# Performance work log

Measured on AMD Instinct MI355X. Metric: run time of the kernel, lower is better.

The kernel has to match this reference:

```python
import jax, jax.numpy as jnp
import numpy as np


def _conv1x1_prelu(x, w, b, a):
    # 1x1 conv == channel matmul; PReLU with shared scalar slope a
    y = jnp.einsum('oc,nchw->nohw', w, x) + b[None, :, None, None]
    return jnp.where(y >= 0, y, a * y)


def setup_inputs() -> dict:
    key = jax.random.key(0)
    ks = jax.random.split(key, 7)
    N, C, H, W = 2, 128, 96, 96
    Ce = 64  # channel // reduction
    s_in = 1.0 / np.sqrt(C)
    return {
        'input': jax.random.normal(ks[0], (N, C, H, W), jnp.float32),
        'w1': jax.random.normal(ks[1], (Ce, C), jnp.float32) * s_in,
        'b1': jnp.zeros((Ce,), jnp.float32),
        'a1': jnp.full((1,), 0.25, jnp.float32),
        'w2': jax.random.normal(ks[2], (Ce, C), jnp.float32) * s_in,
        'b2': jnp.zeros((Ce,), jnp.float32),
        'a2': jnp.full((1,), 0.25, jnp.float32),
        'wa': jax.random.normal(ks[3], (C, C), jnp.float32) * s_in,
        'ba': jnp.zeros((C,), jnp.float32),
        'aa': jnp.full((1,), 0.25, jnp.float32),
    }


def reference(input, w1, b1, a1, w2, b2, a2, wa, ba, aa):
    e1 = _conv1x1_prelu(input, w1, b1, a1[0])  # [N, Ce, H, W]
    e2 = _conv1x1_prelu(input, w2, b2, a2[0])  # [N, Ce, H, W]
    xa = _conv1x1_prelu(input, wa, ba, aa[0])  # [N, C,  H, W]
    N, Ce, H, W = e1.shape
    HW = H * W
    q = e1.transpose(0, 2, 3, 1).reshape(N, HW, Ce)   # [N, HW, Ce]
    k = e2.reshape(N, Ce, HW)                          # [N, Ce, HW]
    score = jax.nn.softmax(jnp.matmul(q, k), axis=-1)  # [N, HW, HW] (no scale, as in source)
    v = xa.reshape(N, -1, HW).transpose(0, 2, 1)       # [N, HW, C]
    out = jnp.matmul(score, v)                         # [N, HW, C]
    return out.transpose(0, 2, 1).reshape(N, -1, H, W)
```

## Files before the change

kernel.cpp:

```cpp
#include <hip/hip_runtime.h>
#include <cstdint>
#include <cstddef>

#define HW_ 9216
#define CC 128
#define NQT 144
#define NQT2 72
#define LOG2E 1.44269504088896f

typedef short bf16x8 __attribute__((ext_vector_type(8)));
typedef unsigned short u16x4 __attribute__((ext_vector_type(4)));
typedef unsigned short u16x8 __attribute__((ext_vector_type(8)));
typedef float f32x4 __attribute__((ext_vector_type(4)));

__device__ __forceinline__ unsigned short f2bf(float f) {
    unsigned int u = __builtin_bit_cast(unsigned int, f);
    u += 0x7FFFu + ((u >> 16) & 1u);
    return (unsigned short)(u >> 16);
}

__device__ __forceinline__ float fast_exp2(float x) {
#if __has_builtin(__builtin_amdgcn_exp2f)
    return __builtin_amdgcn_exp2f(x);
#else
    return exp2f(x);
#endif
}

__device__ __forceinline__ unsigned int cvt_pk_bf16(float lo, float hi) {
    unsigned int r;
    asm("v_cvt_pk_bf16_f32 %0, %1, %2" : "=v"(r) : "v"(lo), "v"(hi));
    return r;
}

__global__ __launch_bounds__(256) void prep_w(const float* __restrict__ w1,
                                              const float* __restrict__ w2,
                                              const float* __restrict__ wa,
                                              float* __restrict__ wt) {
    int idx = blockIdx.x * 256 + threadIdx.x;
    int o = idx >> 7, c = idx & 127;
    float v;
    if (o < 64)       v = w1[o * 128 + c];
    else if (o < 128) v = w2[(o - 64) * 128 + c];
    else              v = wa[(o - 128) * 128 + c];
    wt[c * 256 + o] = v;
}

__global__ __launch_bounds__(256) void conv_kernel(
    const float* __restrict__ x, const float* __restrict__ wt,
    const float* __restrict__ b1, const float* __restrict__ a1,
    const float* __restrict__ b2, const float* __restrict__ a2,
    const float* __restrict__ ba, const float* __restrict__ aa,
    unsigned short* __restrict__ qb, unsigned short* __restrict__ kb,
    unsigned short* __restrict__ vtb) {
    const int ptile = blockIdx.x;
    const int oset  = blockIdx.y;
    const int n     = blockIdx.z;
    const int t = threadIdx.x;
    const int p = t & 63;
    const int og = __builtin_amdgcn_readfirstlane(t >> 6);
    const int p0 = ptile * 64;

    __shared__ float xs[128 * 64];
    for (int c = t >> 6; c < 128; c += 4)
        xs[c * 64 + p] = x[((size_t)n * CC + c) * HW_ + p0 + p];
    __syncthreads();

    const int obase = oset * 64 + og * 16;
    float acc[16];
#pragma unroll
    for (int i = 0; i < 16; i++) acc[i] = 0.f;

    for (int c = 0; c < 128; c++) {
        float xv = xs[c * 64 + p];
        const float* wr = wt + c * 256 + obase;
#pragma unroll
        for (int i = 0; i < 16; i++) acc[i] = fmaf(wr[i], xv, acc[i]);
    }

    const float* bias_p;
    const float* slope_p;
    if (oset == 0)      { bias_p = b1; slope_p = a1; }
    else if (oset == 1) { bias_p = b2; slope_p = a2; }
    else                { bias_p = ba; slope_p = aa; }
    const float slope = slope_p[0];

    unsigned short vals[16];
#pragma unroll
    for (int i = 0; i < 16; i++) {
        float bv = (oset < 2) ? bias_p[og * 16 + i] : bias_p[obase - 128 + i];
        float y = acc[i] + bv;
        y = (y >= 0.f) ? y : slope * y;
        if (oset == 0) y *= LOG2E;
        vals[i] = f2bf(y);
    }

    if (oset < 2) {
        unsigned short* dst = (oset == 0 ? qb : kb) + ((size_t)n * HW_ + p0 + p) * 64 + og * 16;
        bf16x8 v0, v1;
#pragma unroll
        for (int i = 0; i < 8; i++) { v0[i] = (short)vals[i]; v1[i] = (short)vals[8 + i]; }
        *(bf16x8*)(dst)     = v0;
        *(bf16x8*)(dst + 8) = v1;
    } else {
        int c0 = obase - 128;
#pragma unroll
        for (int i = 0; i < 16; i++)
            vtb[((size_t)n * CC + c0 + i) * HW_ + p0 + p] = vals[i];
    }
}

__global__ __launch_bounds__(256, 2) void attn_kernel(
    const unsigned short* __restrict__ qb, const unsigned short* __restrict__ kb,
    const unsigned short* __restrict__ vtb,
    float* __restrict__ o_part, float* __restrict__ l_part,
    int nch, int chunk_j) {
    const int qt    = blockIdx.x;
    const int chunk = blockIdx.y;
    const int n     = blockIdx.z;
    const int t = threadIdx.x;
    const int w = t >> 6;
    const int lane = t & 63;
    const int l15 = lane & 15;
    const int quad = lane >> 4;
    const int e7 = l15 & 7;

    __shared__ __align__(16) unsigned short k_lds[64 * 64];
    __shared__ __align__(16) unsigned short v_lds[128 * 64];
    __shared__ __align__(16) unsigned short p_lds[4 * 1024];

    const int row_ga = qt * 128 + w * 32 + l15;
    const int row_gb = row_ga + 16;
    const bf16x8 bq0a = *(const bf16x8*)(qb + ((size_t)n * HW_ + row_ga) * 64 + quad * 8);
    const bf16x8 bq1a = *(const bf16x8*)(qb + ((size_t)n * HW_ + row_ga) * 64 + 32 + quad * 8);
    const bf16x8 bq0b = *(const bf16x8*)(qb + ((size_t)n * HW_ + row_gb) * 64 + quad * 8);
    const bf16x8 bq1b = *(const bf16x8*)(qb + ((size_t)n * HW_ + row_gb) * 64 + 32 + quad * 8);

    f32x4 acc_oa[8], acc_ob[8];
#pragma unroll
    for (int i = 0; i < 8; i++) {
        acc_oa[i] = (f32x4){0.f, 0.f, 0.f, 0.f};
        acc_ob[i] = (f32x4){0.f, 0.f, 0.f, 0.f};
    }
    float l_sa = 0.f, l_sb = 0.f;

    const int stg_row = t >> 3, stg_seg = t & 7;
    const int iters = chunk_j / 64;
    int j0 = chunk * chunk_j;

    bf16x8 kr0, kr1, vr0, vr1, vr2, vr3;
    {
        const unsigned short* kp = kb + ((size_t)n * HW_ + j0 + stg_row) * 64 + stg_seg * 8;
        kr0 = *(const bf16x8*)kp;
        kr1 = *(const bf16x8*)(kp + 32 * 64);
        const unsigned short* vp = vtb + ((size_t)n * CC + stg_row) * HW_ + j0 + stg_seg * 8;
        vr0 = *(const bf16x8*)vp;
        vr1 = *(const bf16x8*)(vp + (size_t)32 * HW_);
        vr2 = *(const bf16x8*)(vp + (size_t)64 * HW_);
        vr3 = *(const bf16x8*)(vp + (size_t)96 * HW_);
    }

    for (int it = 0; it < iters; ++it, j0 += 64) {
        __syncthreads();
        {
            int r0 = stg_row, r1 = stg_row + 32;
            *(bf16x8*)&k_lds[r0 * 64 + ((stg_seg ^ (r0 & 7)) * 8)] = kr0;
            *(bf16x8*)&k_lds[r1 * 64 + ((stg_seg ^ (r1 & 7)) * 8)] = kr1;
            *(bf16x8*)&v_lds[r0 * 64 + ((stg_seg ^ (r0 & 7)) * 8)] = vr0;
            *(bf16x8*)&v_lds[r1 * 64 + ((stg_seg ^ (r1 & 7)) * 8)] = vr1;
            int r2 = stg_row + 64, r3 = stg_row + 96;
            *(bf16x8*)&v_lds[r2 * 64 + ((stg_seg ^ (r2 & 7)) * 8)] = vr2;
            *(bf16x8*)&v_lds[r3 * 64 + ((stg_seg ^ (r3 & 7)) * 8)] = vr3;
        }
        __syncthreads();

        if (it + 1 < iters) {
            const unsigned short* kp = kb + ((size_t)n * HW_ + j0 + 64 + stg_row) * 64 + stg_seg * 8;
            kr0 = *(const bf16x8*)kp;
            kr1 = *(const bf16x8*)(kp + 32 * 64);
            const unsigned short* vp = vtb + ((size_t)n * CC + stg_row) * HW_ + j0 + 64 + stg_seg * 8;
            vr0 = *(const bf16x8*)vp;
            vr1 = *(const bf16x8*)(vp + (size_t)32 * HW_);
            vr2 = *(const bf16x8*)(vp + (size_t)64 * HW_);
            vr3 = *(const bf16x8*)(vp + (size_t)96 * HW_);
        }

        f32x4 sa[4], sb[4];
#pragma unroll
        for (int ct = 0; ct < 4; ct++) {
            int jr = ct * 16 + l15;
            bf16x8 ak0 = *(const bf16x8*)&k_lds[jr * 64 + ((quad ^ e7) * 8)];
            bf16x8 ak1 = *(const bf16x8*)&k_lds[jr * 64 + (((4 + quad) ^ e7) * 8)];
            f32x4 za = (f32x4){0.f, 0.f, 0.f, 0.f};
            za = __builtin_amdgcn_mfma_f32_16x16x32_bf16(ak0, bq0a, za, 0, 0, 0);
            za = __builtin_amdgcn_mfma_f32_16x16x32_bf16(ak1, bq1a, za, 0, 0, 0);
            sa[ct] = za;
            f32x4 zb = (f32x4){0.f, 0.f, 0.f, 0.f};
            zb = __builtin_amdgcn_mfma_f32_16x16x32_bf16(ak0, bq0b, zb, 0, 0, 0);
            zb = __builtin_amdgcn_mfma_f32_16x16x32_bf16(ak1, bq1b, zb, 0, 0, 0);
            sb[ct] = zb;
        }

#pragma unroll
        for (int ct = 0; ct < 4; ct++) {
            sa[ct][0] = fast_exp2(sa[ct][0]);
            sa[ct][1] = fast_exp2(sa[ct][1]);
            sa[ct][2] = fast_exp2(sa[ct][2]);
            sa[ct][3] = fast_exp2(sa[ct][3]);
        }
        {
            float u0 = sa[0][0] + sa[0][1], u1 = sa[0][2] + sa[0][3];
            float u2 = sa[1][0] + sa[1][1], u3 = sa[1][2] + sa[1][3];
            float u4 = sa[2][0] + sa[2][1], u5 = sa[2][2] + sa[2][3];
            float u6 = sa[3][0] + sa[3][1], u7 = sa[3][2] + sa[3][3];
            float v0 = u0 + u1, v1 = u2 + u3, v2 = u4 + u5, v3 = u6 + u7;
            l_sa += (v0 + v1) + (v2 + v3);
        }
#pragma unroll
        for (int ct = 0; ct < 4; ct++) {
            unsigned int pk01 = cvt_pk_bf16(sa[ct][0], sa[ct][1]);
            unsigned int pk23 = cvt_pk_bf16(sa[ct][2], sa[ct][3]);
            int chunkid = 2 * ct + (quad >> 1);
            int off = l15 * 64 + ((chunkid ^ e7) * 8) + 4 * (quad & 1);
            uint2 tmp;
            tmp.x = pk01;
            tmp.y = pk23;
            *(u16x4*)&p_lds[w * 1024 + off] = __builtin_bit_cast(u16x4, tmp);
        }
        asm volatile("" ::: "memory");
        const bf16x8 bp0a = __builtin_bit_cast(bf16x8,
            *(const u16x8*)&p_lds[w * 1024 + l15 * 64 + ((quad ^ e7) * 8)]);
        const bf16x8 bp1a = __builtin_bit_cast(bf16x8,
            *(const u16x8*)&p_lds[w * 1024 + l15 * 64 + (((4 + quad) ^ e7) * 8)]);
        asm volatile("" ::: "memory");

#pragma unroll
        for (int ct = 0; ct < 4; ct++) {
            sb[ct][0] = fast_exp2(sb[ct][0]);
            sb[ct][1] = fast_exp2(sb[ct][1]);
            sb[ct][2] = fast_exp2(sb[ct][2]);
            sb[ct][3] = fast_exp2(sb[ct][3]);
        }
        {
            float u0 = sb[0][0] + sb[0][1], u1 = sb[0][2] + sb[0][3];
            float u2 = sb[1][0] + sb[1][1], u3 = sb[1][2] + sb[1][3];
            float u4 = sb[2][0] + sb[2][1], u5 = sb[2][2] + sb[2][3];
            float u6 = sb[3][0] + sb[3][1], u7 = sb[3][2] + sb[3][3];
            float v0 = u0 + u1, v1 = u2 + u3, v2 = u4 + u5, v3 = u6 + u7;
            l_sb += (v0 + v1) + (v2 + v3);
        }
#pragma unroll
        for (int ct = 0; ct < 4; ct++) {
            unsigned int pk01 = cvt_pk_bf16(sb[ct][0], sb[ct][1]);
            unsigned int pk23 = cvt_pk_bf16(sb[ct][2], sb[ct][3]);
            int chunkid = 2 * ct + (quad >> 1);
            int off = l15 * 64 + ((chunkid ^ e7) * 8) + 4 * (quad & 1);
            uint2 tmp;
            tmp.x = pk01;
            tmp.y = pk23;
            *(u16x4*)&p_lds[w * 1024 + off] = __builtin_bit_cast(u16x4, tmp);
        }
        asm volatile("" ::: "memory");
        const bf16x8 bp0b = __builtin_bit_cast(bf16x8,
            *(const u16x8*)&p_lds[w * 1024 + l15 * 64 + ((quad ^ e7) * 8)]);
        const bf16x8 bp1b = __builtin_bit_cast(bf16x8,
            *(const u16x8*)&p_lds[w * 1024 + l15 * 64 + (((4 + quad) ^ e7) * 8)]);
        asm volatile("" ::: "memory");

        __builtin_amdgcn_s_setprio(1);
#pragma unroll
        for (int ctv = 0; ctv < 8; ctv++) {
            int cr = ctv * 16 + l15;
            bf16x8 av0 = *(const bf16x8*)&v_lds[cr * 64 + ((quad ^ e7) * 8)];
            bf16x8 av1 = *(const bf16x8*)&v_lds[cr * 64 + (((4 + quad) ^ e7) * 8)];
            acc_oa[ctv] = __builtin_amdgcn_mfma_f32_16x16x32_bf16(av0, bp0a, acc_oa[ctv], 0, 0, 0);
            acc_oa[ctv] = __builtin_amdgcn_mfma_f32_16x16x32_bf16(av1, bp1a, acc_oa[ctv], 0, 0, 0);
            acc_ob[ctv] = __builtin_amdgcn_mfma_f32_16x16x32_bf16(av0, bp0b, acc_ob[ctv], 0, 0, 0);
            acc_ob[ctv] = __builtin_amdgcn_mfma_f32_16x16x32_bf16(av1, bp1b, acc_ob[ctv], 0, 0, 0);
        }
        __builtin_amdgcn_s_setprio(0);
    }

    l_sa += __shfl_xor(l_sa, 16);
    l_sa += __shfl_xor(l_sa, 32);
    l_sb += __shfl_xor(l_sb, 16);
    l_sb += __shfl_xor(l_sb, 32);

    const size_t cbase = ((size_t)(n * NQT2 + qt) * nch + chunk) * 128;
    const int qla = w * 32 + l15, qlb = qla + 16;
#pragma unroll
    for (int ctv = 0; ctv < 8; ctv++)
#pragma unroll
        for (int r = 0; r < 4; r++) {
            int c = ctv * 16 + 4 * quad + r;
            o_part[(cbase + c) * 128 + qla] = acc_oa[ctv][r];
            o_part[(cbase + c) * 128 + qlb] = acc_ob[ctv][r];
        }
    if (quad == 0) {
        size_t lb = ((size_t)(n * NQT2 + qt) * nch + chunk) * 128;
        l_part[lb + qla] = l_sa;
        l_part[lb + qlb] = l_sb;
    }
}

__global__ __launch_bounds__(256) void combine_kernel(
    const float* __restrict__ o_part, const float* __restrict__ lp,
    float* __restrict__ out, int nch) {
    int gid = blockIdx.x * 256 + threadIdx.x;
    int r = gid & 127;
    int rest = gid >> 7;
    int c = rest & 127;
    int nqt = rest >> 7;
    int n = nqt / NQT2, qtp = nqt - n * NQT2;

    float num = 0.f, den = 0.f;
    for (int ch = 0; ch < nch; ch++) {
        num += o_part[(((size_t)nqt * nch + ch) * 128 + c) * 128 + r];
        den += lp[((size_t)nqt * nch + ch) * 128 + r];
    }
    out[((size_t)n * CC + c) * HW_ + qtp * 128 + r] = num / den;
}

extern "C" void kernel_launch(void* const* d_in, const int* in_sizes, int n_in,
                              void* d_out, int out_size, void* d_ws, size_t ws_size,
                              hipStream_t stream) {
    const float* x  = (const float*)d_in[0];
    const float* w1 = (const float*)d_in[1];
    const float* b1 = (const float*)d_in[2];
    const float* a1 = (const float*)d_in[3];
    const float* w2 = (const float*)d_in[4];
    const float* b2 = (const float*)d_in[5];
    const float* a2 = (const float*)d_in[6];
    const float* wa = (const float*)d_in[7];
    const float* ba = (const float*)d_in[8];
    const float* aa = (const float*)d_in[9];
    float* out = (float*)d_out;

    auto need = [](int nc) -> size_t {
        return 9568256ull + (size_t)nc * 9437184ull + (size_t)nc * 73728ull;
    };
    int nch;
    if (ws_size >= need(12))     nch = 12;
    else if (ws_size >= need(8)) nch = 8;
    else if (ws_size >= need(6)) nch = 6;
    else if (ws_size >= need(4)) nch = 4;
    else                         nch = 2;
    const int chunk_j = HW_ / nch;

    char* ws = (char*)d_ws;
    float*          wt     = (float*)(ws + 0);
    unsigned short* qb     = (unsigned short*)(ws + 131072);
    unsigned short* kb     = (unsigned short*)(ws + 2490368);
    unsigned short* vtb    = (unsigned short*)(ws + 4849664);
    float*          o_part = (float*)(ws + 9568256);
    float*          lpart  = (float*)(ws + 9568256 + (size_t)nch * 9437184);

    hipLaunchKernelGGL(prep_w, dim3(128), dim3(256), 0, stream, w1, w2, wa, wt);
    hipLaunchKernelGGL(conv_kernel, dim3(144, 4, 2), dim3(256), 0, stream,
                       x, wt, b1, a1, b2, a2, ba, aa, qb, kb, vtb);
    hipLaunchKernelGGL(attn_kernel, dim3(NQT2, nch, 2), dim3(256), 0, stream,
                       qb, kb, vtb, o_part, lpart, nch, chunk_j);
    hipLaunchKernelGGL(combine_kernel, dim3(2 * NQT2 * 128 * 128 / 256), dim3(256), 0, stream,
                       o_part, lpart, out, nch);
}
```

Baseline: 207.9 us.

## Double query rows per attention block to reuse K/V tiles across 64 rows per wave

Each attention block now covers 256 query rows instead of 128, with every wave handling four 16-row sub-tiles instead of two. Each staged K/V LDS tile is therefore reused across twice as many queries, halving global K/V traffic and staging work per query. In exchange, accumulator registers double (32 f32x4 per thread), launch bounds drop to one block per SM, and the grid halves to 36x nch x 2 blocks. That hurts occupancy and latency hiding and may leave CUs idle. The combine kernel and partial-buffer layout are adjusted for the 256-row tiles.

```diff
diff --git a/kernel.cpp b/kernel.cpp
--- a/kernel.cpp
+++ b/kernel.cpp
@@ -5,7 +5,7 @@
 #define HW_ 9216
 #define CC 128
 #define NQT 144
-#define NQT2 72
+#define NQT4 36
 #define LOG2E 1.44269504088896f
 
 typedef short bf16x8 __attribute__((ext_vector_type(8)));
@@ -110,7 +110,7 @@
     }
 }
 
-__global__ __launch_bounds__(256, 2) void attn_kernel(
+__global__ __launch_bounds__(256, 1) void attn_kernel(
     const unsigned short* __restrict__ qb, const unsigned short* __restrict__ kb,
     const unsigned short* __restrict__ vtb,
     float* __restrict__ o_part, float* __restrict__ l_part,
@@ -127,22 +127,22 @@
 
     __shared__ __align__(16) unsigned short k_lds[64 * 64];
     __shared__ __align__(16) unsigned short v_lds[128 * 64];
-    __shared__ __align__(16) unsigned short p_lds[4 * 1024];
-
-    const int row_ga = qt * 128 + w * 32 + l15;
-    const int row_gb = row_ga + 16;
-    const bf16x8 bq0a = *(const bf16x8*)(qb + ((size_t)n * HW_ + row_ga) * 64 + quad * 8);
-    const bf16x8 bq1a = *(const bf16x8*)(qb + ((size_t)n * HW_ + row_ga) * 64 + 32 + quad * 8);
-    const bf16x8 bq0b = *(const bf16x8*)(qb + ((size_t)n * HW_ + row_gb) * 64 + quad * 8);
-    const bf16x8 bq1b = *(const bf16x8*)(qb + ((size_t)n * HW_ + row_gb) * 64 + 32 + quad * 8);
-
-    f32x4 acc_oa[8], acc_ob[8];
-#pragma unroll
-    for (int i = 0; i < 8; i++) {
-        acc_oa[i] = (f32x4){0.f, 0.f, 0.f, 0.f};
-        acc_ob[i] = (f32x4){0.f, 0.f, 0.f, 0.f};
-    }
-    float l_sa = 0.f, l_sb = 0.f;
+    __shared__ __align__(16) unsigned short p_lds[4 * 4 * 1024];
+
+    bf16x8 bq0[4], bq1[4];
+#pragma unroll
+    for (int s = 0; s < 4; s++) {
+        const int row_g = qt * 256 + w * 64 + s * 16 + l15;
+        bq0[s] = *(const bf16x8*)(qb + ((size_t)n * HW_ + row_g) * 64 + quad * 8);
+        bq1[s] = *(const bf16x8*)(qb + ((size_t)n * HW_ + row_g) * 64 + 32 + quad * 8);
+    }
+
+    f32x4 acc_o[4][8];
+#pragma unroll
+    for (int s = 0; s < 4; s++)
+#pragma unroll
+        for (int i = 0; i < 8; i++) acc_o[s][i] = (f32x4){0.f, 0.f, 0.f, 0.f};
+    float l_s[4] = {0.f, 0.f, 0.f, 0.f};
 
     const int stg_row = t >> 3, stg_seg = t & 7;
     const int iters = chunk_j / 64;
@@ -185,86 +185,40 @@
             vr3 = *(const bf16x8*)(vp + (size_t)96 * HW_);
         }
 
-        f32x4 sa[4], sb[4];
 #pragma unroll
         for (int ct = 0; ct < 4; ct++) {
             int jr = ct * 16 + l15;
             bf16x8 ak0 = *(const bf16x8*)&k_lds[jr * 64 + ((quad ^ e7) * 8)];
             bf16x8 ak1 = *(const bf16x8*)&k_lds[jr * 64 + (((4 + quad) ^ e7) * 8)];
-            f32x4 za = (f32x4){0.f, 0.f, 0.f, 0.f};
-            za = __builtin_amdgcn_mfma_f32_16x16x32_bf16(ak0, bq0a, za, 0, 0, 0);
-            za = __builtin_amdgcn_mfma_f32_16x16x32_bf16(ak1, bq1a, za, 0, 0, 0);
-            sa[ct] = za;
-            f32x4 zb = (f32x4){0.f, 0.f, 0.f, 0.f};
-            zb = __builtin_amdgcn_mfma_f32_16x16x32_bf16(ak0, bq0b, zb, 0, 0, 0);
-            zb = __builtin_amdgcn_mfma_f32_16x16x32_bf16(ak1, bq1b, zb, 0, 0, 0);
-            sb[ct] = zb;
-        }
-
-#pragma unroll
-        for (int ct = 0; ct < 4; ct++) {
-            sa[ct][0] = fast_exp2(sa[ct][0]);
-            sa[ct][1] = fast_exp2(sa[ct][1]);
-            sa[ct][2] = fast_exp2(sa[ct][2]);
-            sa[ct][3] = fast_exp2(sa[ct][3]);
-        }
-        {
-            float u0 = sa[0][0] + sa[0][1], u1 = sa[0][2] + sa[0][3];
-            float u2 = sa[1][0] + sa[1][1], u3 = sa[1][2] + sa[1][3];
-            float u4 = sa[2][0] + sa[2][1], u5 = sa[2][2] + sa[2][3];
-            float u6 = sa[3][0] + sa[3][1], u7 = sa[3][2] + sa[3][3];
-            float v0 = u0 + u1, v1 = u2 + u3, v2 = u4 + u5, v3 = u6 + u7;
-            l_sa += (v0 + v1) + (v2 + v3);
-        }
-#pragma unroll
-        for (int ct = 0; ct < 4; ct++) {
-            unsigned int pk01 = cvt_pk_bf16(sa[ct][0], sa[ct][1]);
-            unsigned int pk23 = cvt_pk_bf16(sa[ct][2], sa[ct][3]);
-            int chunkid = 2 * ct + (quad >> 1);
-            int off = l15 * 64 + ((chunkid ^ e7) * 8) + 4 * (quad & 1);
-            uint2 tmp;
-            tmp.x = pk01;
-            tmp.y = pk23;
-            *(u16x4*)&p_lds[w * 1024 + off] = __builtin_bit_cast(u16x4, tmp);
-        }
+            const int chunkid = 2 * ct + (quad >> 1);
+            const int off = l15 * 64 + ((chunkid ^ e7) * 8) + 4 * (quad & 1);
+#pragma unroll
+            for (int s = 0; s < 4; s++) {
+                f32x4 z = (f32x4){0.f, 0.f, 0.f, 0.f};
+                z = __builtin_amdgcn_mfma_f32_16x16x32_bf16(ak0, bq0[s], z, 0, 0, 0);
+                z = __builtin_amdgcn_mfma_f32_16x16x32_bf16(ak1, bq1[s], z, 0, 0, 0);
+                float p0 = fast_exp2(z[0]);
+                float p1 = fast_exp2(z[1]);
+                float p2 = fast_exp2(z[2]);
+                float p3 = fast_exp2(z[3]);
+                l_s[s] += (p0 + p1) + (p2 + p3);
+                uint2 tmp;
+                tmp.x = cvt_pk_bf16(p0, p1);
+                tmp.y = cvt_pk_bf16(p2, p3);
+                *(u16x4*)&p_lds[(w * 4 + s) * 1024 + off] = __builtin_bit_cast(u16x4, tmp);
+            }
+        }
+
         asm volatile("" ::: "memory");
-        const bf16x8 bp0a = __builtin_bit_cast(bf16x8,
-            *(const u16x8*)&p_lds[w * 1024 + l15 * 64 + ((quad ^ e7) * 8)]);
-        const bf16x8 bp1a = __builtin_bit_cast(bf16x8,
-            *(const u16x8*)&p_lds[w * 1024 + l15 * 64 + (((4 + quad) ^ e7) * 8)]);
-        asm volatile("" ::: "memory");
-
-#pragma unroll
-        for (int ct = 0; ct < 4; ct++) {
-            sb[ct][0] = fast_exp2(sb[ct][0]);
-            sb[ct][1] = fast_exp2(sb[ct][1]);
-            sb[ct][2] = fast_exp2(sb[ct][2]);
-            sb[ct][3] = fast_exp2(sb[ct][3]);
-        }
-        {
-            float u0 = sb[0][0] + sb[0][1], u1 = sb[0][2] + sb[0][3];
-            float u2 = sb[1][0] + sb[1][1], u3 = sb[1][2] + sb[1][3];
-            float u4 = sb[2][0] + sb[2][1], u5 = sb[2][2] + sb[2][3];
-            float u6 = sb[3][0] + sb[3][1], u7 = sb[3][2] + sb[3][3];
-            float v0 = u0 + u1, v1 = u2 + u3, v2 = u4 + u5, v3 = u6 + u7;
-            l_sb += (v0 + v1) + (v2 + v3);
-        }
-#pragma unroll
-        for (int ct = 0; ct < 4; ct++) {
-            unsigned int pk01 = cvt_pk_bf16(sb[ct][0], sb[ct][1]);
-            unsigned int pk23 = cvt_pk_bf16(sb[ct][2], sb[ct][3]);
-            int chunkid = 2 * ct + (quad >> 1);
-            int off = l15 * 64 + ((chunkid ^ e7) * 8) + 4 * (quad & 1);
-            uint2 tmp;
-            tmp.x = pk01;
-            tmp.y = pk23;
-            *(u16x4*)&p_lds[w * 1024 + off] = __builtin_bit_cast(u16x4, tmp);
-        }
-        asm volatile("" ::: "memory");
-        const bf16x8 bp0b = __builtin_bit_cast(bf16x8,
-            *(const u16x8*)&p_lds[w * 1024 + l15 * 64 + ((quad ^ e7) * 8)]);
-        const bf16x8 bp1b = __builtin_bit_cast(bf16x8,
-            *(const u16x8*)&p_lds[w * 1024 + l15 * 64 + (((4 + quad) ^ e7) * 8)]);
+
+        bf16x8 bp0[4], bp1[4];
+#pragma unroll
+        for (int s = 0; s < 4; s++) {
+            bp0[s] = __builtin_bit_cast(bf16x8,
+                *(const u16x8*)&p_lds[(w * 4 + s) * 1024 + l15 * 64 + ((quad ^ e7) * 8)]);
+            bp1[s] = __builtin_bit_cast(bf16x8,
+                *(const u16x8*)&p_lds[(w * 4 + s) * 1024 + l15 * 64 + (((4 + quad) ^ e7) * 8)]);
+        }
         asm volatile("" ::: "memory");
 
         __builtin_amdgcn_s_setprio(1);
@@ -273,33 +227,38 @@
             int cr = ctv * 16 + l15;
             bf16x8 av0 = *(const bf16x8*)&v_lds[cr * 64 + ((quad ^ e7) * 8)];
             bf16x8 av1 = *(const bf16x8*)&v_lds[cr * 64 + (((4 + quad) ^ e7) * 8)];
-            acc_oa[ctv] = __builtin_amdgcn_mfma_f32_16x16x32_bf16(av0, bp0a, acc_oa[ctv], 0, 0, 0);
-            acc_oa[ctv] = __builtin_amdgcn_mfma_f32_16x16x32_bf16(av1, bp1a, acc_oa[ctv], 0, 0, 0);
-            acc_ob[ctv] = __builtin_amdgcn_mfma_f32_16x16x32_bf16(av0, bp0b, acc_ob[ctv], 0, 0, 0);
-            acc_ob[ctv] = __builtin_amdgcn_mfma_f32_16x16x32_bf16(av1, bp1b, acc_ob[ctv], 0, 0, 0);
+#pragma unroll
+            for (int s = 0; s < 4; s++) {
+                acc_o[s][ctv] = __builtin_amdgcn_mfma_f32_16x16x32_bf16(av0, bp0[s], acc_o[s][ctv], 0, 0, 0);
+                acc_o[s][ctv] = __builtin_amdgcn_mfma_f32_16x16x32_bf16(av1, bp1[s], acc_o[s][ctv], 0, 0, 0);
+            }
         }
         __builtin_amdgcn_s_setprio(0);
     }
 
-    l_sa += __shfl_xor(l_sa, 16);
-    l_sa += __shfl_xor(l_sa, 32);
-    l_sb += __shfl_xor(l_sb, 16);
-    l_sb += __shfl_xor(l_sb, 32);
-
-    const size_t cbase = ((size_t)(n * NQT2 + qt) * nch + chunk) * 128;
-    const int qla = w * 32 + l15, qlb = qla + 16;
-#pragma unroll
-    for (int ctv = 0; ctv < 8; ctv++)
-#pragma unroll
-        for (int r = 0; r < 4; r++) {
-            int c = ctv * 16 + 4 * quad + r;
-            o_part[(cbase + c) * 128 + qla] = acc_oa[ctv][r];
-            o_part[(cbase + c) * 128 + qlb] = acc_ob[ctv][r];
-        }
+#pragma unroll
+    for (int s = 0; s < 4; s++) {
+        l_s[s] += __shfl_xor(l_s[s], 16);
+        l_s[s] += __shfl_xor(l_s[s], 32);
+    }
+
+    const size_t cbase = ((size_t)(n * NQT4 + qt) * nch + chunk) * 128;
+#pragma unroll
+    for (int s = 0; s < 4; s++) {
+        const int ql = w * 64 + s * 16 + l15;
+#pragma unroll
+        for (int ctv = 0; ctv < 8; ctv++)
+#pragma unroll
+            for (int r = 0; r < 4; r++) {
+                int c = ctv * 16 + 4 * quad + r;
+                o_part[(cbase + c) * 256 + ql] = acc_o[s][ctv][r];
+            }
+    }
     if (quad == 0) {
-        size_t lb = ((size_t)(n * NQT2 + qt) * nch + chunk) * 128;
-        l_part[lb + qla] = l_sa;
-        l_part[lb + qlb] = l_sb;
+        size_t lb = ((size_t)(n * NQT4 + qt) * nch + chunk) * 256;
+#pragma unroll
+        for (int s = 0; s < 4; s++)
+            l_part[lb + w * 64 + s * 16 + l15] = l_s[s];
     }
 }
 
@@ -307,18 +266,18 @@
     const float* __restrict__ o_part, const float* __restrict__ lp,
     float* __restrict__ out, int nch) {
     int gid = blockIdx.x * 256 + threadIdx.x;
-    int r = gid & 127;
-    int rest = gid >> 7;
+    int r = gid & 255;
+    int rest = gid >> 8;
     int c = rest & 127;
     int nqt = rest >> 7;
-    int n = nqt / NQT2, qtp = nqt - n * NQT2;
+    int n = nqt / NQT4, qtp = nqt - n * NQT4;
 
     float num = 0.f, den = 0.f;
     for (int ch = 0; ch < nch; ch++) {
-        num += o_part[(((size_t)nqt * nch + ch) * 128 + c) * 128 + r];
-        den += lp[((size_t)nqt * nch + ch) * 128 + r];
-    }
-    out[((size_t)n * CC + c) * HW_ + qtp * 128 + r] = num / den;
+        num += o_part[(((size_t)nqt * nch + ch) * 128 + c) * 256 + r];
+        den += lp[((size_t)nqt * nch + ch) * 256 + r];
+    }
+    out[((size_t)n * CC + c) * HW_ + qtp * 256 + r] = num / den;
 }
 
 extern "C" void kernel_launch(void* const* d_in, const int* in_sizes, int n_in,
@@ -358,8 +317,8 @@
     hipLaunchKernelGGL(prep_w, dim3(128), dim3(256), 0, stream, w1, w2, wa, wt);
     hipLaunchKernelGGL(conv_kernel, dim3(144, 4, 2), dim3(256), 0, stream,
                        x, wt, b1, a1, b2, a2, ba, aa, qb, kb, vtb);
-    hipLaunchKernelGGL(attn_kernel, dim3(NQT2, nch, 2), dim3(256), 0, stream,
+    hipLaunchKernelGGL(attn_kernel, dim3(NQT4, nch, 2), dim3(256), 0, stream,
                        qb, kb, vtb, o_part, lpart, nch, chunk_j);
-    hipLaunchKernelGGL(combine_kernel, dim3(2 * NQT2 * 128 * 128 / 256), dim3(256), 0, stream,
+    hipLaunchKernelGGL(combine_kernel, dim3(2 * NQT4 * 128 * 256 / 256), dim3(256), 0, stream,
                        o_part, lpart, out, nch);
 }
```

Measured after the change: 248.1 us. 1.19x slower.
